# Kernel optimization log

Measured on AMD Instinct MI355X. Metric: run time of the kernel, lower is better.

The kernel has to match this reference:

```python
import jax, jax.numpy as jnp
import numpy as np

LOG_2PI = float(np.log(2.0 * np.pi))
LOSS_BETA = 1.0
SIGMA = 1.0
EPS = 1e-6


def setup_inputs() -> dict:
    key = jax.random.key(0)
    z_activations = jax.random.normal(key, (2048, 16, 8), dtype=jnp.float32)
    return {"z_activations": z_activations}


def reference(z_activations):
    N, num_attr, pose_dim = z_activations.shape
    x = z_activations.reshape(N, -1)  # (N, K)
    K = x.shape[1]

    # standardize (torch.std is unbiased, ddof=1)
    mean = jnp.mean(x, axis=0, keepdims=True)
    std = jnp.std(x, axis=0, keepdims=True, ddof=1)
    x = (x - mean) / (std + EPS)

    logN = jnp.log(jnp.asarray(N, dtype=x.dtype))

    # per-dimension pairwise squared differences: (N, N, K)
    d = (x[:, None, :] - x[None, :, :]) ** 2

    # joint: log p(x_i | x_j) for K-dim Gaussian, sigma=1
    sq_dist = jnp.sum(d, axis=2)  # (N, N)
    c_joint = -0.5 * K * LOG_2PI - K * jnp.log(jnp.asarray(SIGMA, dtype=x.dtype))
    log_prob_joint = c_joint - sq_dist / (2.0 * SIGMA ** 2)
    log_q_z_given_x = jax.nn.logsumexp(log_prob_joint, axis=1) - logN  # (N,)

    # marginals: 1-D Gaussian per dim, all K at once (fuses the torch K-loop)
    c_marg = -0.5 * LOG_2PI - jnp.log(jnp.asarray(SIGMA, dtype=x.dtype))
    log_prob_marg = c_marg - d / (2.0 * SIGMA ** 2)  # (N, N, K)
    log_q_z_j = jax.nn.logsumexp(log_prob_marg, axis=1) - logN  # (N, K)
    sum_log_q_z_j = jnp.sum(log_q_z_j, axis=1)  # (N,)

    tc_loss = jnp.mean(log_q_z_given_x - sum_log_q_z_j)
    return tc_loss * LOSS_BETA
```

## Files before the change

kernel.cpp:

```cpp
#include <hip/hip_runtime.h>

#define NROWS 2048
#define KDIM  128
#define TJ    64
#define NCELL 16
#define PORD  10
#define NJBLK 576

typedef float v4f __attribute__((ext_vector_type(4)));

__device__ __forceinline__ float fexp2(float x){ return __builtin_amdgcn_exp2f(x); }
__device__ __forceinline__ float flog2(float x){ return __builtin_amdgcn_logf(x); }

#define CS 0.8493218002880191f

template<int CTRL>
__device__ __forceinline__ float dpp_ror(float v){
  int r = __builtin_amdgcn_update_dpp(0, __builtin_bit_cast(int, v), CTRL, 0xF, 0xF, true);
  return __builtin_bit_cast(float, r);
}

#define OFF_PART   0
#define OFF_ACCUM  8192
#define OFF_JOINT  8448
#define OFF_SLOG   10496
#define OFF_MOM    12544
#define OFF_CTR    33024
#define ZERO_BASE  OFF_JOINT
#define ZERO_LEN   (2048 + 2048 + 20480 + 4)

__device__ __forceinline__ void col_stats_from(float s, float s2, float& scale, float& shift){
  float m = s * (1.f / NROWS);
  float var = fmaxf((s2 - (float)NROWS * m * m) * (1.f / (NROWS - 1)), 0.f);
  scale = 1.f / (sqrtf(var) + 1e-6f);
  shift = -m * scale;
}

__device__ __forceinline__ void quad_stats(const float* __restrict__ accum, int q,
                                           float4& sc, float4& sh){
  const float4 s  = reinterpret_cast<const float4*>(accum)[q];
  const float4 s2 = reinterpret_cast<const float4*>(accum + KDIM)[q];
  const float invN = 1.f / NROWS, invN1 = 1.f / (NROWS - 1);
#define COMP(c) { float m = s.c * invN; \
                  float var = fmaxf((s2.c - (float)NROWS * m * m) * invN1, 0.f); \
                  float sca = CS / (sqrtf(var) + 1e-6f); sc.c = sca; sh.c = -m * sca; }
  COMP(x) COMP(y) COMP(z) COMP(w)
#undef COMP
}

__global__ __launch_bounds__(1024) void tc_stats(const float* __restrict__ x,
                                                 float* __restrict__ ws){
  const int t  = threadIdx.x;
  const int k  = t & 127;
  const int rg = t >> 7;
  const int r0 = blockIdx.x * 64;
  {
    int idx = blockIdx.x * 1024 + t;
    if (idx < ZERO_LEN) ws[ZERO_BASE + idx] = 0.f;
  }
  float s = 0.f, s2 = 0.f;
  #pragma unroll
  for (int it = 0; it < 8; ++it){
    float v = x[(size_t)(r0 + it * 8 + rg) * KDIM + k];
    s += v;
    s2 = fmaf(v, v, s2);
  }
  __shared__ float ls[8][128], ls2[8][128];
  ls[rg][k] = s; ls2[rg][k] = s2;
  __syncthreads();
  if (t < 128){
    float a = 0.f, b = 0.f;
    #pragma unroll
    for (int g = 0; g < 8; ++g){ a += ls[g][t]; b += ls2[g][t]; }
    ws[OFF_PART + blockIdx.x * 256 + t]       = a;
    ws[OFF_PART + blockIdx.x * 256 + 128 + t] = b;
  }
}

__global__ __launch_bounds__(128) void tc_moments(const float* __restrict__ x,
                                                  float* __restrict__ ws){
  const int k   = blockIdx.x >> 4;
  const int seg = blockIdx.x & 15;
  const int t   = threadIdx.x;
  __shared__ float lm[NCELL * PORD];
  lm[t] = 0.f;
  if (t < 32) lm[128 + t] = 0.f;

  float s = 0.f, s2 = 0.f;
  #pragma unroll
  for (int b = 0; b < 32; ++b){
    s  += ws[OFF_PART + b * 256 + k];
    s2 += ws[OFF_PART + b * 256 + 128 + k];
  }
  if (seg == 0 && t == 0){
    ws[OFF_ACCUM + k]       = s;
    ws[OFF_ACCUM + 128 + k] = s2;
  }
  float scale, shift; col_stats_from(s, s2, scale, shift);
  __syncthreads();

  const int row = seg * 128 + t;
  float y = fmaf(x[(size_t)row * KDIM + k], scale, shift);
  int c = (int)floorf(y * 2.f + 8.f);
  c = min(max(c, 0), NCELL - 1);
  float u = y - (-3.75f + 0.5f * (float)c);
  float* b10 = &lm[c * PORD];
  atomicAdd(&b10[0], 1.f);
  float pw = u;
  atomicAdd(&b10[1], pw);
  pw *= u; atomicAdd(&b10[2], pw * 0.5f);
  pw *= u; atomicAdd(&b10[3], pw * 1.6666666666e-1f);
  pw *= u; atomicAdd(&b10[4], pw * 4.1666666666e-2f);
  pw *= u; atomicAdd(&b10[5], pw * 8.3333333333e-3f);
  pw *= u; atomicAdd(&b10[6], pw * 1.3888888889e-3f);
  pw *= u; atomicAdd(&b10[7], pw * 1.9841269841e-4f);
  pw *= u; atomicAdd(&b10[8], pw * 2.4801587302e-5f);
  pw *= u; atomicAdd(&b10[9], pw * 2.7557319224e-6f);
  __syncthreads();

  float* mom = ws + OFF_MOM;
  for (int idx = t; idx < NCELL * PORD; idx += 128){
    int c2 = idx / PORD, m = idx - c2 * PORD;
    atomicAdd(&mom[(size_t)(c2 * KDIM + k) * PORD + m], lm[idx]);
  }
}

__global__ __launch_bounds__(512) void tc_joint(const float* __restrict__ x,
                                                float* __restrict__ ws,
                                                float* __restrict__ out){
  __shared__ float tile[TJ][KDIM];
  __shared__ float colacc[128];
  __shared__ int   lastflag;
  const float* accum = ws + OFF_ACCUM;
  float* joint = ws + OFF_JOINT;
  float* slog  = ws + OFF_SLOG;
  const float* mom = ws + OFF_MOM;

  const int bid  = blockIdx.x;
  const int t    = threadIdx.x;
  const int wave = t >> 6;
  const int lane = t & 63;
  const int g    = lane >> 4;
  const int h    = lane & 15;

  int pair = bid >> 4, sub = (bid >> 1) & 7, jhalf = bid & 1;
  int a = 0, rem = pair;
  while (rem >= 8 - a){ rem -= 8 - a; ++a; }
  const int b = a + rem;
  const int i0 = a * 256 + sub * 32;
  const int j0 = b * 256 + jhalf * 128;
  const bool offdiag = (a != b);

  const int row = i0 + wave * 4 + g;

  if (t < 128) colacc[t] = 0.f;

  const int kq = t & 31;
  float4 sc4, sh4; quad_stats(accum, kq, sc4, sh4);

  v4f xA, xB;
  {
    float4 scA, shA, scB, shB;
    quad_stats(accum, h,      scA, shA);
    quad_stats(accum, 16 + h, scB, shB);
    float4 rA = reinterpret_cast<const float4*>(x + (size_t)row * KDIM)[h];
    float4 rB = reinterpret_cast<const float4*>(x + (size_t)row * KDIM)[16 + h];
    xA = (v4f){fmaf(rA.x, scA.x, shA.x), fmaf(rA.y, scA.y, shA.y),
               fmaf(rA.z, scA.z, shA.z), fmaf(rA.w, scA.w, shA.w)};
    xB = (v4f){fmaf(rB.x, scB.x, shB.x), fmaf(rB.y, scB.y, shB.y),
               fmaf(rB.z, scB.z, shB.z), fmaf(rB.w, scB.w, shB.w)};
  }

  float jacc = 0.f;
  const int jr0 = t >> 5;

  for (int jt = 0; jt < 128; jt += TJ){
    __syncthreads();
    #pragma unroll
    for (int p = 0; p < 4; ++p){
      const int jr = jr0 + 16 * p;
      float4 v = reinterpret_cast<const float4*>(x + (size_t)(j0 + jt + jr) * KDIM)[kq];
      v4f w = {fmaf(v.x, sc4.x, sh4.x), fmaf(v.y, sc4.y, sh4.y),
               fmaf(v.z, sc4.z, sh4.z), fmaf(v.w, sc4.w, sh4.w)};
      *reinterpret_cast<v4f*>(&tile[jr][kq * 4]) = w;
    }
    __syncthreads();

    #pragma unroll 8
    for (int j = 0; j < TJ; ++j){
      const v4f aa = *reinterpret_cast<const v4f*>(&tile[j][4 * h]);
      const v4f bb = *reinterpret_cast<const v4f*>(&tile[j][64 + 4 * h]);
      v4f uA = xA - aa, uB = xB - bb;
      float p0 = uA.x * uA.x, p1 = uA.y * uA.y;
      p0 = fmaf(uA.z, uA.z, p0); p1 = fmaf(uA.w, uA.w, p1);
      p0 = fmaf(uB.x, uB.x, p0); p1 = fmaf(uB.y, uB.y, p1);
      p0 = fmaf(uB.z, uB.z, p0); p1 = fmaf(uB.w, uB.w, p1);
      float pd = p0 + p1;
      pd += dpp_ror<0x121>(pd);
      pd += dpp_ror<0x122>(pd);
      pd += dpp_ror<0x124>(pd);
      pd += dpp_ror<0x128>(pd);
      if (__ballot(pd < 65.f)){
        float e = fexp2(-pd);
        jacc += e;
        if (offdiag && h == 0) atomicAdd(&colacc[jt + j], e);
      }
    }
  }

  if (h == 0) atomicAdd(&joint[row], jacc);
  __syncthreads();
  if (offdiag && t < 128){
    float c = colacc[t];
    if (c != 0.f) atomicAdd(&joint[j0 + t], c);
  }

  if (bid < 512){
    const int k  = t & 127;
    const int ir = t >> 7;
    const int r  = bid * 4 + ir;
    float scale, shift;
    col_stats_from(accum[k], accum[128 + k], scale, shift);
    const float y = fmaf(x[(size_t)r * KDIM + k], scale, shift);
    float S = 0.f;
    #pragma unroll
    for (int c = 0; c < NCELL; ++c){
      const float* mp = mom + (size_t)(c * KDIM + k) * PORD;
      float q0 = mp[0], q1 = mp[1], q2 = mp[2], q3 = mp[3], q4 = mp[4];
      float q5 = mp[5], q6 = mp[6], q7 = mp[7], q8 = mp[8], q9 = mp[9];
      float s  = y - (-3.75f + 0.5f * (float)c);
      float scl = s * CS;
      float e  = fexp2(-(scl * scl));
      float prev = 1.f, cur = s, nxt;
      float inner = fmaf(q1, s, q0);
      nxt = fmaf(s, cur, -prev);        inner = fmaf(q2, nxt, inner); prev = cur; cur = nxt;
      nxt = fmaf(s, cur, -2.f * prev);  inner = fmaf(q3, nxt, inner); prev = cur; cur = nxt;
      nxt = fmaf(s, cur, -3.f * prev);  inner = fmaf(q4, nxt, inner); prev = cur; cur = nxt;
      nxt = fmaf(s, cur, -4.f * prev);  inner = fmaf(q5, nxt, inner); prev = cur; cur = nxt;
      nxt = fmaf(s, cur, -5.f * prev);  inner = fmaf(q6, nxt, inner); prev = cur; cur = nxt;
      nxt = fmaf(s, cur, -6.f * prev);  inner = fmaf(q7, nxt, inner); prev = cur; cur = nxt;
      nxt = fmaf(s, cur, -7.f * prev);  inner = fmaf(q8, nxt, inner); prev = cur; cur = nxt;
      nxt = fmaf(s, cur, -8.f * prev);  inner = fmaf(q9, nxt, inner);
      S = fmaf(e, inner, S);
    }
    float lg = flog2(S);
    #pragma unroll
    for (int off = 1; off < 64; off <<= 1) lg += __shfl_xor(lg, off);
    if (lane == 0) atomicAdd(&slog[r], lg);
  }

  __syncthreads();
  if (t == 0){
    __threadfence();
    unsigned int* ctr = (unsigned int*)(ws + OFF_CTR);
    unsigned int old = __hip_atomic_fetch_add(ctr, 1u, __ATOMIC_ACQ_REL, __HIP_MEMORY_SCOPE_AGENT);
    lastflag = (old == NJBLK - 1);
  }
  __syncthreads();
  if (lastflag){
    __shared__ float red[8];
    float acc = 0.f;
    #pragma unroll
    for (int q = 0; q < 4; ++q){
      int r = q * 512 + t;
      float jv = __hip_atomic_load(&joint[r], __ATOMIC_RELAXED, __HIP_MEMORY_SCOPE_AGENT);
      float sv = __hip_atomic_load(&slog[r],  __ATOMIC_RELAXED, __HIP_MEMORY_SCOPE_AGENT);
      acc += 0.6931471805599453f * (flog2(jv) - sv);
    }
    #pragma unroll
    for (int off = 1; off < 64; off <<= 1) acc += __shfl_xor(acc, off);
    if (lane == 0) red[wave] = acc;
    __syncthreads();
    if (t == 0){
      float tot = 0.f;
      #pragma unroll
      for (int w2 = 0; w2 < 8; ++w2) tot += red[w2];
      out[0] = tot * (1.0f / NROWS) + 968.32661124224364f;
    }
  }
}

extern "C" void kernel_launch(void* const* d_in, const int* in_sizes, int n_in,
                              void* d_out, int out_size, void* d_ws, size_t ws_size,
                              hipStream_t stream){
  const float* x = (const float*)d_in[0];
  float* out = (float*)d_out;
  float* ws  = (float*)d_ws;

  tc_stats  <<<32, 1024, 0, stream>>>(x, ws);
  tc_moments<<<KDIM * 16, 128, 0, stream>>>(x, ws);
  tc_joint  <<<NJBLK, 512, 0, stream>>>(x, ws, out);
}
```

Measured before the change: 116.4 us.

## Compute joint pairwise distances via bf16 MFMA Gram matrix with precomputed norms

Standardized, pre-scaled activations are written as bf16 into the workspace by the moments kernel. The joint kernel then tiles 128x64 row blocks into swizzled LDS and computes dot products with 16x16x32 bf16 MFMA, forming squared distances as norm_i + norm_j - 2*dot. This replaces the scalar per-pair difference loop, which used symmetric triangular tiling and early-exit ballots. It removes most of the VALU work in exchange for bf16 rounding error, the cancellation risk inherent in the norm expansion, and evaluating the full non-symmetric grid.

Result: slower. 124.1 us (+6.6%).

```diff
diff --git a/kernel.cpp b/kernel.cpp
--- a/kernel.cpp
+++ b/kernel.cpp
@@ -1,24 +1,19 @@
 #include <hip/hip_runtime.h>
+#include <hip/hip_bf16.h>
 
 #define NROWS 2048
 #define KDIM  128
-#define TJ    64
 #define NCELL 16
 #define PORD  10
-#define NJBLK 576
-
-typedef float v4f __attribute__((ext_vector_type(4)));
+#define NJBLK 512
+
+typedef float f32x4  __attribute__((ext_vector_type(4)));
+typedef short bf16x8 __attribute__((ext_vector_type(8)));
 
 __device__ __forceinline__ float fexp2(float x){ return __builtin_amdgcn_exp2f(x); }
 __device__ __forceinline__ float flog2(float x){ return __builtin_amdgcn_logf(x); }
 
 #define CS 0.8493218002880191f
-
-template<int CTRL>
-__device__ __forceinline__ float dpp_ror(float v){
-  int r = __builtin_amdgcn_update_dpp(0, __builtin_bit_cast(int, v), CTRL, 0xF, 0xF, true);
-  return __builtin_bit_cast(float, r);
-}
 
 #define OFF_PART   0
 #define OFF_ACCUM  8192
@@ -26,6 +21,7 @@
 #define OFF_SLOG   10496
 #define OFF_MOM    12544
 #define OFF_CTR    33024
+#define OFF_XS     33028
 #define ZERO_BASE  OFF_JOINT
 #define ZERO_LEN   (2048 + 2048 + 20480 + 4)
 
@@ -34,18 +30,6 @@
   float var = fmaxf((s2 - (float)NROWS * m * m) * (1.f / (NROWS - 1)), 0.f);
   scale = 1.f / (sqrtf(var) + 1e-6f);
   shift = -m * scale;
-}
-
-__device__ __forceinline__ void quad_stats(const float* __restrict__ accum, int q,
-                                           float4& sc, float4& sh){
-  const float4 s  = reinterpret_cast<const float4*>(accum)[q];
-  const float4 s2 = reinterpret_cast<const float4*>(accum + KDIM)[q];
-  const float invN = 1.f / NROWS, invN1 = 1.f / (NROWS - 1);
-#define COMP(c) { float m = s.c * invN; \
-                  float var = fmaxf((s2.c - (float)NROWS * m * m) * invN1, 0.f); \
-                  float sca = CS / (sqrtf(var) + 1e-6f); sc.c = sca; sh.c = -m * sca; }
-  COMP(x) COMP(y) COMP(z) COMP(w)
-#undef COMP
 }
 
 __global__ __launch_bounds__(1024) void tc_stats(const float* __restrict__ x,
@@ -101,6 +85,12 @@
 
   const int row = seg * 128 + t;
   float y = fmaf(x[(size_t)row * KDIM + k], scale, shift);
+
+  {
+    __hip_bfloat16 hb = __float2bfloat16(y * CS);
+    ((unsigned short*)(ws + OFF_XS))[(size_t)row * KDIM + k] = *(unsigned short*)&hb;
+  }
+
   int c = (int)floorf(y * 2.f + 8.f);
   c = min(max(c, 0), NCELL - 1);
   float u = y - (-3.75f + 0.5f * (float)c);
@@ -128,94 +118,108 @@
 __global__ __launch_bounds__(512) void tc_joint(const float* __restrict__ x,
                                                 float* __restrict__ ws,
                                                 float* __restrict__ out){
-  __shared__ float tile[TJ][KDIM];
-  __shared__ float colacc[128];
-  __shared__ int   lastflag;
-  const float* accum = ws + OFF_ACCUM;
+  __shared__ __align__(16) char ls[49152];
+  __shared__ float nI[128], nJ[64];
+  __shared__ float red2[8];
+  __shared__ int lastflag;
+
+  const int t = threadIdx.x;
+  const int wave = t >> 6, lane = t & 63;
+  const int bid = blockIdx.x;
+  const int bi = bid >> 5, bj = bid & 31;
+  const int Ibase = bi * 128, Jbase = bj * 64;
   float* joint = ws + OFF_JOINT;
   float* slog  = ws + OFF_SLOG;
-  const float* mom = ws + OFF_MOM;
-
-  const int bid  = blockIdx.x;
-  const int t    = threadIdx.x;
-  const int wave = t >> 6;
-  const int lane = t & 63;
-  const int g    = lane >> 4;
-  const int h    = lane & 15;
-
-  int pair = bid >> 4, sub = (bid >> 1) & 7, jhalf = bid & 1;
-  int a = 0, rem = pair;
-  while (rem >= 8 - a){ rem -= 8 - a; ++a; }
-  const int b = a + rem;
-  const int i0 = a * 256 + sub * 32;
-  const int j0 = b * 256 + jhalf * 128;
-  const bool offdiag = (a != b);
-
-  const int row = i0 + wave * 4 + g;
-
-  if (t < 128) colacc[t] = 0.f;
-
-  const int kq = t & 31;
-  float4 sc4, sh4; quad_stats(accum, kq, sc4, sh4);
-
-  v4f xA, xB;
+  const float* accum = ws + OFF_ACCUM;
+  const float* mom   = ws + OFF_MOM;
+  const unsigned short* xs = (const unsigned short*)(ws + OFF_XS);
+
+  #pragma unroll
+  for (int q = 0; q < 4; ++q){
+    int g = t + q * 512;
+    int row = g >> 4, c16 = g & 15;
+    uint4 v = *(const uint4*)(xs + (size_t)(Ibase + row) * KDIM + c16 * 8);
+    *(uint4*)(ls + row * 256 + ((c16 * 16) ^ ((row & 7) << 4))) = v;
+  }
+  #pragma unroll
+  for (int q = 0; q < 2; ++q){
+    int g = t + q * 512;
+    int row = g >> 4, c16 = g & 15;
+    uint4 v = *(const uint4*)(xs + (size_t)(Jbase + row) * KDIM + c16 * 8);
+    *(uint4*)(ls + 32768 + row * 256 + ((c16 * 16) ^ ((row & 7) << 4))) = v;
+  }
+  __syncthreads();
+
+  if (t < 192){
+    int row = (t < 128) ? t : (t - 128);
+    const char* base = (t < 128) ? ls : (ls + 32768);
+    float n = 0.f;
+    #pragma unroll
+    for (int g2 = 0; g2 < 16; ++g2){
+      uint4 v = *(const uint4*)(base + row * 256 + ((g2 * 16) ^ ((row & 7) << 4)));
+      const unsigned int* u = (const unsigned int*)&v;
+      #pragma unroll
+      for (int e = 0; e < 4; ++e){
+        float lo = __builtin_bit_cast(float, u[e] << 16);
+        float hi = __builtin_bit_cast(float, u[e] & 0xFFFF0000u);
+        n = fmaf(lo, lo, n); n = fmaf(hi, hi, n);
+      }
+    }
+    if (t < 128) nI[row] = n; else nJ[row] = n;
+  }
+  __syncthreads();
+
+  const int wi = wave >> 2, wj = wave & 3;
+  const int mrow0 = wi * 64 + (lane & 15);
+  const int nrow  = wj * 16 + (lane & 15);
+  f32x4 acc0 = {0.f,0.f,0.f,0.f}, acc1 = acc0, acc2 = acc0, acc3 = acc0;
+  #pragma unroll
+  for (int kq = 0; kq < 4; ++kq){
+    const int boff = kq * 64 + (lane >> 4) * 16;
+    const int mx = (mrow0 & 7) << 4;
+    bf16x8 bf = *(const bf16x8*)(ls + 32768 + nrow * 256 + (boff ^ ((nrow & 7) << 4)));
+    bf16x8 a0 = *(const bf16x8*)(ls + (mrow0 +  0) * 256 + (boff ^ mx));
+    bf16x8 a1 = *(const bf16x8*)(ls + (mrow0 + 16) * 256 + (boff ^ mx));
+    bf16x8 a2 = *(const bf16x8*)(ls + (mrow0 + 32) * 256 + (boff ^ mx));
+    bf16x8 a3 = *(const bf16x8*)(ls + (mrow0 + 48) * 256 + (boff ^ mx));
+    acc0 = __builtin_amdgcn_mfma_f32_16x16x32_bf16(a0, bf, acc0, 0, 0, 0);
+    acc1 = __builtin_amdgcn_mfma_f32_16x16x32_bf16(a1, bf, acc1, 0, 0, 0);
+    acc2 = __builtin_amdgcn_mfma_f32_16x16x32_bf16(a2, bf, acc2, 0, 0, 0);
+    acc3 = __builtin_amdgcn_mfma_f32_16x16x32_bf16(a3, bf, acc3, 0, 0, 0);
+  }
+
+  const float njv = nJ[nrow];
+  const int rbase = (lane >> 4) * 4;
+  float jp[4][4];
+  #pragma unroll
+  for (int mt = 0; mt < 4; ++mt){
+    f32x4 a4 = (mt == 0) ? acc0 : (mt == 1) ? acc1 : (mt == 2) ? acc2 : acc3;
+    #pragma unroll
+    for (int p = 0; p < 4; ++p){
+      int iloc = wi * 64 + mt * 16 + rbase + p;
+      float pd = nI[iloc] + njv - 2.f * a4[p];
+      jp[mt][p] = fexp2(-pd);
+    }
+  }
+  #pragma unroll
+  for (int mt = 0; mt < 4; ++mt){
+    #pragma unroll
+    for (int p = 0; p < 4; ++p){
+      float v = jp[mt][p];
+      v += __shfl_xor(v, 1); v += __shfl_xor(v, 2);
+      v += __shfl_xor(v, 4); v += __shfl_xor(v, 8);
+      jp[mt][p] = v;
+    }
+  }
+  if ((lane & 15) == 0){
+    #pragma unroll
+    for (int mt = 0; mt < 4; ++mt)
+      #pragma unroll
+      for (int p = 0; p < 4; ++p)
+        atomicAdd(&joint[Ibase + wi * 64 + mt * 16 + rbase + p], jp[mt][p]);
+  }
+
   {
-    float4 scA, shA, scB, shB;
-    quad_stats(accum, h,      scA, shA);
-    quad_stats(accum, 16 + h, scB, shB);
-    float4 rA = reinterpret_cast<const float4*>(x + (size_t)row * KDIM)[h];
-    float4 rB = reinterpret_cast<const float4*>(x + (size_t)row * KDIM)[16 + h];
-    xA = (v4f){fmaf(rA.x, scA.x, shA.x), fmaf(rA.y, scA.y, shA.y),
-               fmaf(rA.z, scA.z, shA.z), fmaf(rA.w, scA.w, shA.w)};
-    xB = (v4f){fmaf(rB.x, scB.x, shB.x), fmaf(rB.y, scB.y, shB.y),
-               fmaf(rB.z, scB.z, shB.z), fmaf(rB.w, scB.w, shB.w)};
-  }
-
-  float jacc = 0.f;
-  const int jr0 = t >> 5;
-
-  for (int jt = 0; jt < 128; jt += TJ){
-    __syncthreads();
-    #pragma unroll
-    for (int p = 0; p < 4; ++p){
-      const int jr = jr0 + 16 * p;
-      float4 v = reinterpret_cast<const float4*>(x + (size_t)(j0 + jt + jr) * KDIM)[kq];
-      v4f w = {fmaf(v.x, sc4.x, sh4.x), fmaf(v.y, sc4.y, sh4.y),
-               fmaf(v.z, sc4.z, sh4.z), fmaf(v.w, sc4.w, sh4.w)};
-      *reinterpret_cast<v4f*>(&tile[jr][kq * 4]) = w;
-    }
-    __syncthreads();
-
-    #pragma unroll 8
-    for (int j = 0; j < TJ; ++j){
-      const v4f aa = *reinterpret_cast<const v4f*>(&tile[j][4 * h]);
-      const v4f bb = *reinterpret_cast<const v4f*>(&tile[j][64 + 4 * h]);
-      v4f uA = xA - aa, uB = xB - bb;
-      float p0 = uA.x * uA.x, p1 = uA.y * uA.y;
-      p0 = fmaf(uA.z, uA.z, p0); p1 = fmaf(uA.w, uA.w, p1);
-      p0 = fmaf(uB.x, uB.x, p0); p1 = fmaf(uB.y, uB.y, p1);
-      p0 = fmaf(uB.z, uB.z, p0); p1 = fmaf(uB.w, uB.w, p1);
-      float pd = p0 + p1;
-      pd += dpp_ror<0x121>(pd);
-      pd += dpp_ror<0x122>(pd);
-      pd += dpp_ror<0x124>(pd);
-      pd += dpp_ror<0x128>(pd);
-      if (__ballot(pd < 65.f)){
-        float e = fexp2(-pd);
-        jacc += e;
-        if (offdiag && h == 0) atomicAdd(&colacc[jt + j], e);
-      }
-    }
-  }
-
-  if (h == 0) atomicAdd(&joint[row], jacc);
-  __syncthreads();
-  if (offdiag && t < 128){
-    float c = colacc[t];
-    if (c != 0.f) atomicAdd(&joint[j0 + t], c);
-  }
-
-  if (bid < 512){
     const int k  = t & 127;
     const int ir = t >> 7;
     const int r  = bid * 4 + ir;
@@ -228,19 +232,19 @@
       const float* mp = mom + (size_t)(c * KDIM + k) * PORD;
       float q0 = mp[0], q1 = mp[1], q2 = mp[2], q3 = mp[3], q4 = mp[4];
       float q5 = mp[5], q6 = mp[6], q7 = mp[7], q8 = mp[8], q9 = mp[9];
-      float s  = y - (-3.75f + 0.5f * (float)c);
-      float scl = s * CS;
+      float sC  = y - (-3.75f + 0.5f * (float)c);
+      float scl = sC * CS;
       float e  = fexp2(-(scl * scl));
-      float prev = 1.f, cur = s, nxt;
-      float inner = fmaf(q1, s, q0);
-      nxt = fmaf(s, cur, -prev);        inner = fmaf(q2, nxt, inner); prev = cur; cur = nxt;
-      nxt = fmaf(s, cur, -2.f * prev);  inner = fmaf(q3, nxt, inner); prev = cur; cur = nxt;
-      nxt = fmaf(s, cur, -3.f * prev);  inner = fmaf(q4, nxt, inner); prev = cur; cur = nxt;
-      nxt = fmaf(s, cur, -4.f * prev);  inner = fmaf(q5, nxt, inner); prev = cur; cur = nxt;
-      nxt = fmaf(s, cur, -5.f * prev);  inner = fmaf(q6, nxt, inner); prev = cur; cur = nxt;
-      nxt = fmaf(s, cur, -6.f * prev);  inner = fmaf(q7, nxt, inner); prev = cur; cur = nxt;
-      nxt = fmaf(s, cur, -7.f * prev);  inner = fmaf(q8, nxt, inner); prev = cur; cur = nxt;
-      nxt = fmaf(s, cur, -8.f * prev);  inner = fmaf(q9, nxt, inner);
+      float prev = 1.f, cur = sC, nxt;
+      float inner = fmaf(q1, sC, q0);
+      nxt = fmaf(sC, cur, -1.f * prev); inner = fmaf(q2, nxt, inner); prev = cur; cur = nxt;
+      nxt = fmaf(sC, cur, -2.f * prev); inner = fmaf(q3, nxt, inner); prev = cur; cur = nxt;
+      nxt = fmaf(sC, cur, -3.f * prev); inner = fmaf(q4, nxt, inner); prev = cur; cur = nxt;
+      nxt = fmaf(sC, cur, -4.f * prev); inner = fmaf(q5, nxt, inner); prev = cur; cur = nxt;
+      nxt = fmaf(sC, cur, -5.f * prev); inner = fmaf(q6, nxt, inner); prev = cur; cur = nxt;
+      nxt = fmaf(sC, cur, -6.f * prev); inner = fmaf(q7, nxt, inner); prev = cur; cur = nxt;
+      nxt = fmaf(sC, cur, -7.f * prev); inner = fmaf(q8, nxt, inner); prev = cur; cur = nxt;
+      nxt = fmaf(sC, cur, -8.f * prev); inner = fmaf(q9, nxt, inner);
       S = fmaf(e, inner, S);
     }
     float lg = flog2(S);
@@ -258,7 +262,6 @@
   }
   __syncthreads();
   if (lastflag){
-    __shared__ float red[8];
     float acc = 0.f;
     #pragma unroll
     for (int q = 0; q < 4; ++q){
@@ -268,13 +271,13 @@
       acc += 0.6931471805599453f * (flog2(jv) - sv);
     }
     #pragma unroll
-    for (int off = 1; off < 64; off <<= 1) acc += __shfl_xor(acc, off);
-    if (lane == 0) red[wave] = acc;
+    for (int m = 1; m < 64; m <<= 1) acc += __shfl_xor(acc, m);
+    if (lane == 0) red2[wave] = acc;
     __syncthreads();
     if (t == 0){
       float tot = 0.f;
       #pragma unroll
-      for (int w2 = 0; w2 < 8; ++w2) tot += red[w2];
+      for (int w = 0; w < 8; ++w) tot += red2[w];
       out[0] = tot * (1.0f / NROWS) + 968.32661124224364f;
     }
   }
@@ -286,7 +289,6 @@
   const float* x = (const float*)d_in[0];
   float* out = (float*)d_out;
   float* ws  = (float*)d_ws;
-
   tc_stats  <<<32, 1024, 0, stream>>>(x, ws);
   tc_moments<<<KDIM * 16, 128, 0, stream>>>(x, ws);
   tc_joint  <<<NJBLK, 512, 0, stream>>>(x, ws, out);
```
